# Kernel optimization log

Hardware: AMD Instinct MI355X
Metric: run time of the kernel (lower is better)

## Reference

```python
import jax, jax.numpy as jnp
import numpy as np

A = 0.7071067811865476  # sqrt(2)/2
B_ = 1.0 - A
KH = KW = 3
K2 = 9
STRIDE = 1
PAD = 1
DIL = 1


def setup_inputs() -> dict:
    key = jax.random.key(0)
    k1, k2, k3, k4 = jax.random.split(key, 4)
    Bn, Cin, H, W = 4, 256, 64, 64
    Cout = 256
    x = jax.random.normal(k1, (Bn, Cin, H, W), dtype=jnp.float32)
    offset = jax.random.normal(k2, (Bn, 2 * K2, H, W), dtype=jnp.float32)
    mask = jax.random.uniform(k3, (Bn, K2, H, W), dtype=jnp.float32)
    stdv = 1.0 / np.sqrt(Cin * KH * KW)
    weight = jax.random.uniform(k4, (Cout, Cin, KH, KW), dtype=jnp.float32,
                                minval=-stdv, maxval=stdv)
    bias = jnp.zeros((Cout,), dtype=jnp.float32)
    return {"input": x, "offset": offset, "mask": mask, "weight": weight, "bias": bias}


def _weight_circle(weight):
    # Blend 3x3 corner taps along the diagonal "circle", as in DCNv2_Circle.forward.
    O, C = weight.shape[0], weight.shape[1]
    w = weight.reshape(O, C, K2)
    w0 = A * (A * w[:, :, 0] + B_ * w[:, :, 1]) + B_ * (A * w[:, :, 3] + B_ * w[:, :, 4])
    w2 = A * (B_ * w[:, :, 1] + A * w[:, :, 2]) + B_ * (B_ * w[:, :, 4] + A * w[:, :, 5])
    w6 = B_ * (A * w[:, :, 3] + B_ * w[:, :, 4]) + A * (A * w[:, :, 6] + B_ * w[:, :, 7])
    w8 = B_ * (B_ * w[:, :, 4] + A * w[:, :, 5]) + A * (B_ * w[:, :, 7] + A * w[:, :, 8])
    return jnp.stack([w0, w[:, :, 1], w2, w[:, :, 3], w[:, :, 4],
                      w[:, :, 5], w6, w[:, :, 7], w8], axis=-1)  # [O, C, 9]


def _dcn_v2(x, offset, mask, w_flat, bias):
    Bn, C, H, W = x.shape
    Ho = (H + 2 * PAD - DIL * (KH - 1) - 1) // STRIDE + 1
    Wo = (W + 2 * PAD - DIL * (KW - 1) - 1) // STRIDE + 1
    # Base sampling grid per kernel tap k: [K2, Ho, Wo]
    ki, kj = jnp.meshgrid(jnp.arange(KH), jnp.arange(KW), indexing="ij")
    ki = ki.reshape(K2).astype(jnp.float32)
    kj = kj.reshape(K2).astype(jnp.float32)
    oy = (jnp.arange(Ho, dtype=jnp.float32) * STRIDE - PAD)
    ox = (jnp.arange(Wo, dtype=jnp.float32) * STRIDE - PAD)
    base_y = oy[None, :, None] + DIL * ki[:, None, None]  # [K2, Ho, 1]
    base_x = ox[None, None, :] + DIL * kj[:, None, None]  # [K2, 1, Wo]
    # Offsets: channel 2k is dy, 2k+1 is dx (DCNv2 layout).
    off = offset.reshape(Bn, K2, 2, Ho, Wo)
    y = base_y[None] + off[:, :, 0]  # [B, K2, Ho, Wo]
    x_ = base_x[None] + off[:, :, 1]
    y0 = jnp.floor(y)
    x0 = jnp.floor(x_)
    ly = y - y0
    lx = x_ - x0
    y0i = y0.astype(jnp.int32)
    x0i = x0.astype(jnp.int32)
    flat = x.reshape(Bn, C, H * W)

    def gather(yi, xi):
        valid = (yi >= 0) & (yi < H) & (xi >= 0) & (xi < W)
        idx = jnp.clip(yi, 0, H - 1) * W + jnp.clip(xi, 0, W - 1)  # [B,K2,Ho,Wo]
        v = jax.vmap(lambda f, i: f[:, i.reshape(-1)])(flat, idx)  # [B,C,K2*Ho*Wo]
        v = v.reshape(Bn, C, K2, Ho, Wo)
        return v * valid[:, None].astype(v.dtype)

    hy = 1.0 - ly
    hx = 1.0 - lx
    # corner weights broadcast over channel dim
    sampled = (gather(y0i, x0i) * (hy * hx)[:, None]
               + gather(y0i, x0i + 1) * (hy * lx)[:, None]
               + gather(y0i + 1, x0i) * (ly * hx)[:, None]
               + gather(y0i + 1, x0i + 1) * (ly * lx)[:, None])  # [B,C,K2,Ho,Wo]
    sampled = sampled * mask[:, None]  # modulation
    out = jnp.einsum("bckhw,ock->bohw", sampled, w_flat)
    return out + bias[None, :, None, None]


def reference(input, offset, mask, weight, bias):
    w_flat = _weight_circle(weight)
    return _dcn_v2(input, offset, mask, w_flat, bias)
```

## Files before the change

kernel.cpp:

```cpp
#include <hip/hip_runtime.h>

typedef __bf16 bf16x8 __attribute__((ext_vector_type(8)));
typedef float f32x4 __attribute__((ext_vector_type(4)));

#define HH 64
#define WW 64
#define HW 4096
#define COUT 256
#define NROWS 12
#define BS_SZ 37888
#define XS_OFF 75776
#define XS_SZ 24576
#define SMEM_SZ 124928

__device__ __forceinline__ void bar_sync() {
    asm volatile("s_waitcnt lgkmcnt(0)" ::: "memory");
    __builtin_amdgcn_s_barrier();
    asm volatile("" ::: "memory");
}
__device__ __forceinline__ void bar_sync_vm() {
    asm volatile("s_waitcnt vmcnt(0) lgkmcnt(0)" ::: "memory");
    __builtin_amdgcn_s_barrier();
    asm volatile("" ::: "memory");
}

__global__ __launch_bounds__(256) void prep(const float* __restrict__ weight,
                                            const float* __restrict__ x,
                                            __bf16* __restrict__ wp,
                                            __bf16* __restrict__ xs) {
    __shared__ float ws[2304];
    const int tid = threadIdx.x;
    if (blockIdx.x < 2048) {
        const int bh = blockIdx.x >> 3;
        const int u  = ((blockIdx.x & 7) << 8) + tid;
        const int b = bh >> 6, h = bh & 63;
        const float* xr = x + (size_t)b * 256 * HW + h * 64;
        const int gsg = u >> 6, w = u & 63;
        bf16x8 v;
        #pragma unroll
        for (int c8 = 0; c8 < 8; ++c8)
            v[c8] = (__bf16)xr[(size_t)(gsg * 8 + c8) * HW + w];
        *(bf16x8*)&xs[(size_t)bh * 16384 + (size_t)u * 8] = v;
        return;
    }
    const int o = blockIdx.x - 2048;
    const float4* src = (const float4*)(weight + (size_t)o * 2304);
    float4* dst = (float4*)ws;
    #pragma unroll
    for (int i = 0; i < 3; ++i) {
        int idx = i * 256 + tid;
        if (idx < 576) dst[idx] = src[idx];
    }
    __syncthreads();
    const float Af = 0.70710678118654752f;
    const float Bf = 1.0f - Af;
    const int tm = o >> 4, rr = o & 15;
    for (int fid = tid; fid < 288; fid += 256) {
        const int cgtap = fid >> 2, q = fid & 3;
        const int cg = cgtap / 9, tap = cgtap - 9 * cg;
        const int c0 = cg * 32 + q * 8;
        bf16x8 v;
        #pragma unroll
        for (int j = 0; j < 8; ++j) {
            const float* w = ws + (c0 + j) * 9;
            float r;
            switch (tap) {
                case 0:  r = Af*(Af*w[0]+Bf*w[1]) + Bf*(Af*w[3]+Bf*w[4]); break;
                case 1:  r = w[1]; break;
                case 2:  r = Af*(Bf*w[1]+Af*w[2]) + Bf*(Bf*w[4]+Af*w[5]); break;
                case 3:  r = w[3]; break;
                case 4:  r = w[4]; break;
                case 5:  r = w[5]; break;
                case 6:  r = Bf*(Af*w[3]+Bf*w[4]) + Af*(Af*w[6]+Bf*w[7]); break;
                case 7:  r = w[7]; break;
                default: r = Bf*(Bf*w[4]+Af*w[5]) + Af*(Bf*w[7]+Af*w[8]); break;
            }
            v[j] = (__bf16)r;
        }
        *(bf16x8*)&wp[(size_t)(((cg * 9 + tap) * 16 + tm) * 64 + q * 16 + rr) << 3] = v;
    }
}

__device__ __forceinline__ void mfma_part(const __bf16* __restrict__ wp,
        const char* BsR, int klbeg, int tb, int te, int tm0, int lane,
        int q, int rr, int pcg, f32x4 acc[4][4]) {
    const __bf16* ap = wp + ((size_t)((pcg * 9 + klbeg + tb) * 16 + tm0) * 64 + lane) * 8;
    bf16x8 a0 = *(const bf16x8*)ap;
    bf16x8 a1 = *(const bf16x8*)(ap + 512);
    bf16x8 a2 = *(const bf16x8*)(ap + 1024);
    bf16x8 a3 = *(const bf16x8*)(ap + 1536);
    int kc = ((klbeg + tb) * 32 + q * 8) * 2;
    #pragma unroll 1
    for (int t = tb; t < te; ++t) {
        bf16x8 n0 = a0, n1 = a1, n2 = a2, n3 = a3;
        if (t + 1 < te) {
            const __bf16* np = ap + 8192;
            n0 = *(const bf16x8*)np;
            n1 = *(const bf16x8*)(np + 512);
            n2 = *(const bf16x8*)(np + 1024);
            n3 = *(const bf16x8*)(np + 1536);
        }
        const char* bp = BsR + rr * 592 + kc;
        bf16x8 bb0 = *(const bf16x8*)(bp);
        bf16x8 bb1 = *(const bf16x8*)(bp + 16 * 592);
        bf16x8 bb2 = *(const bf16x8*)(bp + 32 * 592);
        bf16x8 bb3 = *(const bf16x8*)(bp + 48 * 592);
        acc[0][0] = __builtin_amdgcn_mfma_f32_16x16x32_bf16(a0, bb0, acc[0][0], 0, 0, 0);
        acc[1][0] = __builtin_amdgcn_mfma_f32_16x16x32_bf16(a1, bb0, acc[1][0], 0, 0, 0);
        acc[2][0] = __builtin_amdgcn_mfma_f32_16x16x32_bf16(a2, bb0, acc[2][0], 0, 0, 0);
        acc[3][0] = __builtin_amdgcn_mfma_f32_16x16x32_bf16(a3, bb0, acc[3][0], 0, 0, 0);
        acc[0][1] = __builtin_amdgcn_mfma_f32_16x16x32_bf16(a0, bb1, acc[0][1], 0, 0, 0);
        acc[1][1] = __builtin_amdgcn_mfma_f32_16x16x32_bf16(a1, bb1, acc[1][1], 0, 0, 0);
        acc[2][1] = __builtin_amdgcn_mfma_f32_16x16x32_bf16(a2, bb1, acc[2][1], 0, 0, 0);
        acc[3][1] = __builtin_amdgcn_mfma_f32_16x16x32_bf16(a3, bb1, acc[3][1], 0, 0, 0);
        acc[0][2] = __builtin_amdgcn_mfma_f32_16x16x32_bf16(a0, bb2, acc[0][2], 0, 0, 0);
        acc[1][2] = __builtin_amdgcn_mfma_f32_16x16x32_bf16(a1, bb2, acc[1][2], 0, 0, 0);
        acc[2][2] = __builtin_amdgcn_mfma_f32_16x16x32_bf16(a2, bb2, acc[2][2], 0, 0, 0);
        acc[3][2] = __builtin_amdgcn_mfma_f32_16x16x32_bf16(a3, bb2, acc[3][2], 0, 0, 0);
        acc[0][3] = __builtin_amdgcn_mfma_f32_16x16x32_bf16(a0, bb3, acc[0][3], 0, 0, 0);
        acc[1][3] = __builtin_amdgcn_mfma_f32_16x16x32_bf16(a1, bb3, acc[1][3], 0, 0, 0);
        acc[2][3] = __builtin_amdgcn_mfma_f32_16x16x32_bf16(a2, bb3, acc[2][3], 0, 0, 0);
        acc[3][3] = __builtin_amdgcn_mfma_f32_16x16x32_bf16(a3, bb3, acc[3][3], 0, 0, 0);
        ap += 8192;
        kc += 64;
        a0 = n0; a1 = n1; a2 = n2; a3 = n3;
    }
}

__global__ __launch_bounds__(512, 2) void dcn_main(
        const float* __restrict__ x, const float* __restrict__ off,
        const float* __restrict__ msk, const __bf16* __restrict__ wp,
        const __bf16* __restrict__ xs, const float* __restrict__ bias,
        float* __restrict__ out) {
    __shared__ __align__(16) char smem[SMEM_SZ];
    const int tid  = threadIdx.x;
    const int wv   = tid >> 6;
    const int lane = tid & 63;
    const int q    = lane >> 4, rr = lane & 15;
    const int px   = lane;

    const int bid = blockIdx.x;
    const int xcd = bid & 7;
    const int b   = xcd >> 1;
    const int h   = ((xcd & 1) << 5) | (bid >> 3);

    const int rowbase = min(max(h - 5, 0), HH - NROWS);
    const float* xb = x + (size_t)b * 256 * HW;
    const char* xsb = (const char*)xs;

    size_t SB[3]; int XDR[3];
    #pragma unroll
    for (int k = 0; k < 3; ++k) {
        int t = wv * 3 + k;
        int row = t >> 1, sgh = t & 1;
        SB[k]  = (size_t)(b * 64 + rowbase + row) * 32768 + (size_t)(sgh * 1024 + lane * 16);
        XDR[k] = row * 2048 + sgh * 1024;
    }

    float W00[3], W01[3], W10[3], W11[3];
    int AY0[3], AY1[3], DXO[3], COLB[3], GP[3];
    bool UV[3];
    #pragma unroll
    for (int k = 0; k < 3; ++k) {
        int c = (k < 2) ? (wv + 8 * k) : ((wv >= 6) ? wv + 10 : -1);
        UV[k] = (c >= 0);
        if (UV[k]) {
            int sg = c / 9, tap = c % 9;
            int ki = tap / 3, kj = tap - 3 * ki;
            const float* offp = off + (size_t)b * 18 * HW + h * 64 + px;
            float dy = offp[(2 * tap) * HW];
            float dx = offp[(2 * tap + 1) * HW];
            float mv = msk[(size_t)b * 9 * HW + (size_t)tap * HW + h * 64 + px];
            float py  = (float)(h - 1 + ki) + dy;
            float pxf = (float)(px - 1 + kj) + dx;
            float y0f = floorf(py), x0f = floorf(pxf);
            float ly = py - y0f, lx = pxf - x0f;
            float hy = 1.0f - ly, hx = 1.0f - lx;
            int y0 = (int)y0f, x0 = (int)x0f;
            int y1 = y0 + 1, x1 = x0 + 1;
            bool vy0 = (y0 >= 0) && (y0 < HH), vy1 = (y1 >= 0) && (y1 < HH);
            bool vx0 = (x0 >= 0) && (x0 < WW), vx1 = (x1 >= 0) && (x1 < WW);
            int cy0 = min(max(y0, 0), HH - 1), cy1 = min(max(y1, 0), HH - 1);
            int cx0 = min(max(x0, 0), WW - 1), cx1 = min(max(x1, 0), WW - 1);
            W00[k] = (vy0 && vx0) ? hy * hx * mv : 0.0f;
            W01[k] = (vy0 && vx1) ? hy * lx * mv : 0.0f;
            W10[k] = (vy1 && vx0) ? ly * hx * mv : 0.0f;
            W11[k] = (vy1 && vx1) ? ly * lx * mv : 0.0f;
            int ry0 = min(max(cy0 - rowbase, 0), NROWS - 1);
            int ry1 = min(max(cy1 - rowbase, 0), NROWS - 1);
            bool useG = (vy0 && (cy0 < rowbase || cy0 > rowbase + NROWS - 1))
                     || (vy1 && (cy1 < rowbase || cy1 > rowbase + NROWS - 1));
            AY0[k]  = ry0 * 2048 + sg * 1024 + cx0 * 16;
            AY1[k]  = ry1 * 2048 + sg * 1024 + cx0 * 16;
            DXO[k]  = (cx1 - cx0) * 16;
            COLB[k] = (tap * 32 + sg * 8) * 2;
            GP[k]   = cy0 | (cy1 << 6) | (cx0 << 12) | (cx1 << 18) | (sg << 24)
                    | (useG ? (1u << 31) : 0);
        }
    }

    f32x4 acc[4][4];
    #pragma unroll
    for (int i = 0; i < 4; ++i)
        #pragma unroll
        for (int n = 0; n < 4; ++n)
            acc[i][n] = (f32x4)0.0f;

    const int tm0   = (wv & 3) * 4;
    const int klbeg = (wv & 4) ? 5 : 0;
    const int nkl   = (wv & 4) ? 4 : 5;
    const int thalf = (nkl + 1) >> 1;

    #pragma unroll
    for (int k = 0; k < 3; ++k)
        __builtin_amdgcn_global_load_lds(
            (const __attribute__((address_space(1))) void*)(xsb + SB[k]),
            (__attribute__((address_space(3))) void*)(smem + XS_OFF + XDR[k]), 16, 0, 0);

    #pragma unroll 1
    for (int s = 0; s < 16; ++s) {
        const int cg = s >> 1, half = s & 1;
        bar_sync_vm();
        if (s < 15) {
            const int xoff = XS_OFF + ((s + 1) & 1) * XS_SZ;
            #pragma unroll
            for (int k = 0; k < 3; ++k)
                __builtin_amdgcn_global_load_lds(
                    (const __attribute__((address_space(1))) void*)(xsb + SB[k] + (size_t)(s + 1) * 2048),
                    (__attribute__((address_space(3))) void*)(smem + xoff + XDR[k]), 16, 0, 0);
        }
        {
            const char* XsB = (const char*)smem + XS_OFF + (s & 1) * XS_SZ;
            char* BsW = smem + (cg & 1) * BS_SZ;
            #pragma unroll
            for (int k = 0; k < 3; ++k) {
                if (UV[k]) {
                    bf16x8 c00 = *(const bf16x8*)(XsB + AY0[k]);
                    bf16x8 c01 = *(const bf16x8*)(XsB + AY0[k] + DXO[k]);
                    bf16x8 c10 = *(const bf16x8*)(XsB + AY1[k]);
                    bf16x8 c11 = *(const bf16x8*)(XsB + AY1[k] + DXO[k]);
                    float w0 = W00[k], w1 = W01[k], w2 = W10[k], w3 = W11[k];
                    bf16x8 res;
                    #pragma unroll
                    for (int j = 0; j < 8; ++j) {
                        float v = w0 * (float)c00[j] + w1 * (float)c01[j]
                                + w2 * (float)c10[j] + w3 * (float)c11[j];
                        res[j] = (__bf16)v;
                    }
                    int gp = GP[k];
                    if (gp < 0) {
                        int cy0 = gp & 63, cy1 = (gp >> 6) & 63;
                        int cx0 = (gp >> 12) & 63, cx1 = (gp >> 18) & 63;
                        int sg = (gp >> 24) & 3;
                        const float* xc = xb + (size_t)(cg * 32 + half * 16 + sg * 8) * HW;
                        int i00 = cy0 * 64 + cx0, i01 = cy0 * 64 + cx1;
                        int i10 = cy1 * 64 + cx0, i11 = cy1 * 64 + cx1;
                        #pragma unroll
                        for (int j = 0; j < 8; ++j) {
                            float v = w0 * xc[i00] + w1 * xc[i01]
                                    + w2 * xc[i10] + w3 * xc[i11];
                            res[j] = (__bf16)v;
                            xc += HW;
                        }
                    }
                    *(bf16x8*)(BsW + px * 592 + COLB[k] + half * 32) = res;
                }
            }
        }
        if (s >= 2) {
            const int pcg = cg - 1;
            const char* BsR = (const char*)smem + (pcg & 1) * BS_SZ;
            const int tb = half ? thalf : 0;
            const int te = half ? nkl : thalf;
            mfma_part(wp, BsR, klbeg, tb, te, tm0, lane, q, rr, pcg, acc);
        }
    }

    bar_sync();
    mfma_part(wp, (const char*)smem + BS_SZ, klbeg, 0, nkl, tm0, lane, q, rr, 7, acc);

    float* scr = (float*)smem;
    bar_sync();
    if (wv >= 4) {
        const int base = (wv - 4) * 4096 + lane * 4;
        #pragma unroll
        for (int i = 0; i < 4; ++i)
            #pragma unroll
            for (int n = 0; n < 4; ++n)
                *(f32x4*)&scr[base + (i * 4 + n) * 256] = acc[i][n];
    }
    bar_sync();
    if (wv < 4) {
        const int mrow = wv * 64;
        const int base = wv * 4096 + lane * 4;
        #pragma unroll
        for (int i = 0; i < 4; ++i) {
            #pragma unroll
            for (int n = 0; n < 4; ++n) {
                f32x4 p = *(const f32x4*)&scr[base + (i * 4 + n) * 256];
                #pragma unroll
                for (int e = 0; e < 4; ++e) {
                    int m = mrow + i * 16 + q * 4 + e;
                    out[((size_t)b * COUT + m) * HW + h * 64 + n * 16 + rr]
                        = acc[i][n][e] + p[e] + bias[m];
                }
            }
        }
    }
}

extern "C" void kernel_launch(void* const* d_in, const int* in_sizes, int n_in,
                              void* d_out, int out_size, void* d_ws, size_t ws_size,
                              hipStream_t stream) {
    const float* x      = (const float*)d_in[0];
    const float* off    = (const float*)d_in[1];
    const float* msk    = (const float*)d_in[2];
    const float* weight = (const float*)d_in[3];
    const float* bias   = (const float*)d_in[4];
    float* out = (float*)d_out;

    __bf16* wp = (__bf16*)d_ws;
    __bf16* xs = (__bf16*)((char*)d_ws + 1179648);

    prep<<<2304, 256, 0, stream>>>(weight, x, wp, xs);
    dcn_main<<<256, 512, 0, stream>>>(x, off, msk, wp, xs, bias, out);
}
```

Measured before the change: 128.3 us.

## Use 1024-thread blocks with a four-way K split and staged reduction

Raises the block to 16 waves and launch bounds to (1024,1). The nine K steps are split across four wave groups (3,2,2,2 steps) instead of two, and the gather/DMA work is spread over more waves. The partial accumulators are combined through LDS in three serialized rounds, each with two barriers. The register double-buffering of A-operand loads in the MFMA loop is removed, so each iteration now loads its A fragments directly, which may expose global-load latency.

After: 160.9 us. 25.4% more time.

```diff
diff --git a/kernel.cpp b/kernel.cpp
--- a/kernel.cpp
+++ b/kernel.cpp
@@ -82,25 +82,16 @@
 }
 
 __device__ __forceinline__ void mfma_part(const __bf16* __restrict__ wp,
-        const char* BsR, int klbeg, int tb, int te, int tm0, int lane,
+        const char* BsR, int tb, int te, int tm0, int lane,
         int q, int rr, int pcg, f32x4 acc[4][4]) {
-    const __bf16* ap = wp + ((size_t)((pcg * 9 + klbeg + tb) * 16 + tm0) * 64 + lane) * 8;
-    bf16x8 a0 = *(const bf16x8*)ap;
-    bf16x8 a1 = *(const bf16x8*)(ap + 512);
-    bf16x8 a2 = *(const bf16x8*)(ap + 1024);
-    bf16x8 a3 = *(const bf16x8*)(ap + 1536);
-    int kc = ((klbeg + tb) * 32 + q * 8) * 2;
     #pragma unroll 1
     for (int t = tb; t < te; ++t) {
-        bf16x8 n0 = a0, n1 = a1, n2 = a2, n3 = a3;
-        if (t + 1 < te) {
-            const __bf16* np = ap + 8192;
-            n0 = *(const bf16x8*)np;
-            n1 = *(const bf16x8*)(np + 512);
-            n2 = *(const bf16x8*)(np + 1024);
-            n3 = *(const bf16x8*)(np + 1536);
-        }
-        const char* bp = BsR + rr * 592 + kc;
+        const __bf16* ap = wp + ((size_t)((pcg * 9 + t) * 16 + tm0) * 64 + lane) * 8;
+        bf16x8 a0 = *(const bf16x8*)ap;
+        bf16x8 a1 = *(const bf16x8*)(ap + 512);
+        bf16x8 a2 = *(const bf16x8*)(ap + 1024);
+        bf16x8 a3 = *(const bf16x8*)(ap + 1536);
+        const char* bp = BsR + rr * 592 + t * 64 + q * 16;
         bf16x8 bb0 = *(const bf16x8*)(bp);
         bf16x8 bb1 = *(const bf16x8*)(bp + 16 * 592);
         bf16x8 bb2 = *(const bf16x8*)(bp + 32 * 592);
@@ -121,13 +112,10 @@
         acc[1][3] = __builtin_amdgcn_mfma_f32_16x16x32_bf16(a1, bb3, acc[1][3], 0, 0, 0);
         acc[2][3] = __builtin_amdgcn_mfma_f32_16x16x32_bf16(a2, bb3, acc[2][3], 0, 0, 0);
         acc[3][3] = __builtin_amdgcn_mfma_f32_16x16x32_bf16(a3, bb3, acc[3][3], 0, 0, 0);
-        ap += 8192;
-        kc += 64;
-        a0 = n0; a1 = n1; a2 = n2; a3 = n3;
-    }
-}
-
-__global__ __launch_bounds__(512, 2) void dcn_main(
+    }
+}
+
+__global__ __launch_bounds__(1024, 1) void dcn_main(
         const float* __restrict__ x, const float* __restrict__ off,
         const float* __restrict__ msk, const __bf16* __restrict__ wp,
         const __bf16* __restrict__ xs, const float* __restrict__ bias,
@@ -148,23 +136,25 @@
     const float* xb = x + (size_t)b * 256 * HW;
     const char* xsb = (const char*)xs;
 
-    size_t SB[3]; int XDR[3];
-    #pragma unroll
-    for (int k = 0; k < 3; ++k) {
-        int t = wv * 3 + k;
-        int row = t >> 1, sgh = t & 1;
-        SB[k]  = (size_t)(b * 64 + rowbase + row) * 32768 + (size_t)(sgh * 1024 + lane * 16);
-        XDR[k] = row * 2048 + sgh * 1024;
-    }
-
-    float W00[3], W01[3], W10[3], W11[3];
-    int AY0[3], AY1[3], DXO[3], COLB[3], GP[3];
-    bool UV[3];
-    #pragma unroll
-    for (int k = 0; k < 3; ++k) {
-        int c = (k < 2) ? (wv + 8 * k) : ((wv >= 6) ? wv + 10 : -1);
-        UV[k] = (c >= 0);
-        if (UV[k]) {
+    int SB[2], XDR[2];
+    #pragma unroll
+    for (int k = 0; k < 2; ++k) {
+        int t = wv + 16 * k;
+        if (t < 24) {
+            int row = t >> 1, sgh = t & 1;
+            SB[k]  = (b * 64 + rowbase + row) * 32768 + sgh * 1024 + lane * 16;
+            XDR[k] = row * 2048 + sgh * 1024;
+        }
+    }
+    const bool dma1 = (wv < 8);
+
+    const bool u1 = (wv >= 14);
+    float W00[2], W01[2], W10[2], W11[2];
+    int AY0[2], AY1[2], DXO[2], COLB[2], GP[2];
+    #pragma unroll
+    for (int k = 0; k < 2; ++k) {
+        if (k == 0 || u1) {
+            int c = (k == 0) ? wv : 16 + (wv - 14);
             int sg = c / 9, tap = c % 9;
             int ki = tap / 3, kj = tap - 3 * ki;
             const float* offp = off + (size_t)b * 18 * HW + h * 64 + px;
@@ -206,16 +196,18 @@
         for (int n = 0; n < 4; ++n)
             acc[i][n] = (f32x4)0.0f;
 
-    const int tm0   = (wv & 3) * 4;
-    const int klbeg = (wv & 4) ? 5 : 0;
-    const int nkl   = (wv & 4) ? 4 : 5;
-    const int thalf = (nkl + 1) >> 1;
-
-    #pragma unroll
-    for (int k = 0; k < 3; ++k)
-        __builtin_amdgcn_global_load_lds(
-            (const __attribute__((address_space(1))) void*)(xsb + SB[k]),
-            (__attribute__((address_space(3))) void*)(smem + XS_OFF + XDR[k]), 16, 0, 0);
+    const int tm0 = (wv & 3) * 4;
+    const int kg  = wv >> 2;
+    const int klb = (kg == 0) ? 0 : (kg * 2 + 1);
+    const int kle = klb + ((kg == 0) ? 3 : 2);
+    const int tmid = klb + ((kle - klb + 1) >> 1);
+
+    #pragma unroll
+    for (int k = 0; k < 2; ++k)
+        if (k == 0 || dma1)
+            __builtin_amdgcn_global_load_lds(
+                (const __attribute__((address_space(1))) void*)(xsb + SB[k]),
+                (__attribute__((address_space(3))) void*)(smem + XS_OFF + XDR[k]), 16, 0, 0);
 
     #pragma unroll 1
     for (int s = 0; s < 16; ++s) {
@@ -224,17 +216,18 @@
         if (s < 15) {
             const int xoff = XS_OFF + ((s + 1) & 1) * XS_SZ;
             #pragma unroll
-            for (int k = 0; k < 3; ++k)
-                __builtin_amdgcn_global_load_lds(
-                    (const __attribute__((address_space(1))) void*)(xsb + SB[k] + (size_t)(s + 1) * 2048),
-                    (__attribute__((address_space(3))) void*)(smem + xoff + XDR[k]), 16, 0, 0);
+            for (int k = 0; k < 2; ++k)
+                if (k == 0 || dma1)
+                    __builtin_amdgcn_global_load_lds(
+                        (const __attribute__((address_space(1))) void*)(xsb + SB[k] + (s + 1) * 2048),
+                        (__attribute__((address_space(3))) void*)(smem + xoff + XDR[k]), 16, 0, 0);
         }
         {
             const char* XsB = (const char*)smem + XS_OFF + (s & 1) * XS_SZ;
             char* BsW = smem + (cg & 1) * BS_SZ;
             #pragma unroll
-            for (int k = 0; k < 3; ++k) {
-                if (UV[k]) {
+            for (int k = 0; k < 2; ++k) {
+                if (k == 0 || u1) {
                     bf16x8 c00 = *(const bf16x8*)(XsB + AY0[k]);
                     bf16x8 c01 = *(const bf16x8*)(XsB + AY0[k] + DXO[k]);
                     bf16x8 c10 = *(const bf16x8*)(XsB + AY1[k]);
@@ -270,39 +263,51 @@
         if (s >= 2) {
             const int pcg = cg - 1;
             const char* BsR = (const char*)smem + (pcg & 1) * BS_SZ;
-            const int tb = half ? thalf : 0;
-            const int te = half ? nkl : thalf;
-            mfma_part(wp, BsR, klbeg, tb, te, tm0, lane, q, rr, pcg, acc);
+            const int tb = half ? tmid : klb;
+            const int te = half ? kle : tmid;
+            mfma_part(wp, BsR, tb, te, tm0, lane, q, rr, pcg, acc);
         }
     }
 
     bar_sync();
-    mfma_part(wp, (const char*)smem + BS_SZ, klbeg, 0, nkl, tm0, lane, q, rr, 7, acc);
+    mfma_part(wp, (const char*)smem + BS_SZ, klb, kle, tm0, lane, q, rr, 7, acc);
 
     float* scr = (float*)smem;
     bar_sync();
-    if (wv >= 4) {
-        const int base = (wv - 4) * 4096 + lane * 4;
-        #pragma unroll
-        for (int i = 0; i < 4; ++i)
-            #pragma unroll
-            for (int n = 0; n < 4; ++n)
-                *(f32x4*)&scr[base + (i * 4 + n) * 256] = acc[i][n];
-    }
-    bar_sync();
-    if (wv < 4) {
+    #pragma unroll 1
+    for (int r = 1; r <= 3; ++r) {
+        if (kg == r) {
+            const int base = (wv & 3) * 4096 + lane * 4;
+            #pragma unroll
+            for (int i = 0; i < 4; ++i)
+                #pragma unroll
+                for (int n = 0; n < 4; ++n)
+                    *(f32x4*)&scr[base + (i * 4 + n) * 256] = acc[i][n];
+        }
+        bar_sync();
+        if (kg == 0) {
+            const int base = wv * 4096 + lane * 4;
+            #pragma unroll
+            for (int i = 0; i < 4; ++i)
+                #pragma unroll
+                for (int n = 0; n < 4; ++n) {
+                    f32x4 p = *(const f32x4*)&scr[base + (i * 4 + n) * 256];
+                    acc[i][n] += p;
+                }
+        }
+        bar_sync();
+    }
+    if (kg == 0) {
         const int mrow = wv * 64;
-        const int base = wv * 4096 + lane * 4;
         #pragma unroll
         for (int i = 0; i < 4; ++i) {
             #pragma unroll
             for (int n = 0; n < 4; ++n) {
-                f32x4 p = *(const f32x4*)&scr[base + (i * 4 + n) * 256];
                 #pragma unroll
                 for (int e = 0; e < 4; ++e) {
                     int m = mrow + i * 16 + q * 4 + e;
                     out[((size_t)b * COUT + m) * HW + h * 64 + n * 16 + rr]
-                        = acc[i][n][e] + p[e] + bias[m];
+                        = acc[i][n][e] + bias[m];
                 }
             }
         }
@@ -323,5 +328,5 @@
     __bf16* xs = (__bf16*)((char*)d_ws + 1179648);
 
     prep<<<2304, 256, 0, stream>>>(weight, x, wp, xs);
-    dcn_main<<<256, 512, 0, stream>>>(x, off, msk, wp, xs, bias, out);
-}
+    dcn_main<<<256, 1024, 0, stream>>>(x, off, msk, wp, xs, bias, out);
+}
```
